# Kernel optimization log

Hardware: AMD Instinct MI355X
Metric: run time of the kernel (lower is better)

The kernel has to match this reference:

```python
import jax, jax.numpy as jnp
import numpy as np

LN_EPS = 1e-5
RMS_EPS = 1e-5

B, T, D = 4, 2048, 1024
H, DK, DV = 4, 256, 512            # head_k_dim = D/H, head_v_dim = expand_v * head_k_dim (expand_v=2)
KDIM, VDIM = H * DK, H * DV        # 1024, 2048
FFN = 4096                          # int(d_model * ffn_ratio)
CONV = 4


def _layernorm(x, w, b):
    mu = jnp.mean(x, -1, keepdims=True)
    var = jnp.mean(jnp.square(x - mu), -1, keepdims=True)
    return (x - mu) * jax.lax.rsqrt(var + LN_EPS) * w + b


def _short_conv_silu(x, w):
    # causal depthwise conv, kernel size K, then SiLU. x: [B,T,C], w: [C,K]
    K = w.shape[1]
    xp = jnp.pad(x, ((0, 0), (K - 1, 0), (0, 0)))
    y = sum(xp[:, i:i + x.shape[1], :] * w[:, i] for i in range(K))
    return jax.nn.silu(y)


def _l2norm(x):
    return x * jax.lax.rsqrt(jnp.sum(jnp.square(x), -1, keepdims=True) + 1e-6)


def _gated_delta_rule(q, k, v, g, beta):
    # q,k: [B,T,H,DK]; v: [B,T,H,DV]; g,beta: [B,T,H]
    # S_t = exp(g_t)*S_{t-1} + k_t (beta_t*(v_t - k_t^T exp(g_t) S_{t-1}))^T ; o_t = q_t^T S_t
    def step(S, inp):
        qt, kt, vt, gt, bt = inp
        S = S * jnp.exp(gt)[..., None, None]          # [B,H,DK,DV]
        mem = jnp.einsum('bhk,bhkv->bhv', kt, S)
        delta = (vt - mem) * bt[..., None]
        S = S + jnp.einsum('bhk,bhv->bhkv', kt, delta)
        o = jnp.einsum('bhk,bhkv->bhv', qt, S)
        return S, o
    S0 = jnp.zeros((q.shape[0], H, DK, DV), q.dtype)
    xs = (q.transpose(1, 0, 2, 3), k.transpose(1, 0, 2, 3), v.transpose(1, 0, 2, 3),
          g.transpose(1, 0, 2), beta.transpose(1, 0, 2))
    _, o = jax.lax.scan(step, S0, xs)
    return o.transpose(1, 0, 2, 3)  # [B,T,H,DV]


def setup_inputs() -> dict:
    key = jax.random.key(0)
    ks = jax.random.split(key, 24)
    n = lambda k, shp, s=0.02: jax.random.normal(k, shp, dtype=jnp.float32) * s
    return {
        'x': jax.random.normal(ks[0], (B, T, D), dtype=jnp.float32),
        'Wq': n(ks[1], (D, KDIM)), 'Wk': n(ks[2], (D, KDIM)), 'Wv': n(ks[3], (D, VDIM)),
        'Wa': n(ks[4], (D, H)), 'Wb': n(ks[5], (D, H)), 'Wg': n(ks[6], (D, VDIM)),
        'conv_q_w': n(ks[7], (KDIM, CONV), 0.2), 'conv_k_w': n(ks[8], (KDIM, CONV), 0.2),
        'conv_v_w': n(ks[9], (VDIM, CONV), 0.2),
        'A_log': jnp.log(jax.random.uniform(ks[10], (H,), minval=1.0, maxval=16.0, dtype=jnp.float32)),
        'dt_bias': jax.random.uniform(ks[11], (H,), minval=0.0, maxval=0.5, dtype=jnp.float32),
        'o_norm_w': jnp.ones((DV,), jnp.float32),
        'Wo': n(ks[12], (VDIM, D)),
        'ln1_w': jnp.ones((D,), jnp.float32), 'ln1_b': jnp.zeros((D,), jnp.float32),
        'ln2_w': jnp.ones((D,), jnp.float32), 'ln2_b': jnp.zeros((D,), jnp.float32),
        'ffn_w1': n(ks[13], (D, FFN)), 'ffn_b1': jnp.zeros((FFN,), jnp.float32),
        'ffn_w2': n(ks[14], (FFN, D)), 'ffn_b2': jnp.zeros((D,), jnp.float32),
    }


def reference(x, Wq, Wk, Wv, Wa, Wb, Wg, conv_q_w, conv_k_w, conv_v_w, A_log, dt_bias,
              o_norm_w, Wo, ln1_w, ln1_b, ln2_w, ln2_b, ffn_w1, ffn_b1, ffn_w2, ffn_b2):
    normed = _layernorm(x, ln1_w, ln1_b)
    q = _short_conv_silu(normed @ Wq, conv_q_w).reshape(B, T, H, DK)
    k = _short_conv_silu(normed @ Wk, conv_k_w).reshape(B, T, H, DK)
    v = _short_conv_silu(normed @ Wv, conv_v_w).reshape(B, T, H, DV)
    q = _l2norm(q) * (DK ** -0.5)
    k = _l2norm(k)
    g = -jnp.exp(A_log) * jax.nn.softplus(normed @ Wa + dt_bias)   # [B,T,H], negative
    beta = jax.nn.sigmoid(normed @ Wb)                              # [B,T,H]
    o = _gated_delta_rule(q, k, v, g, beta)                         # [B,T,H,DV]
    gate = (normed @ Wg).reshape(B, T, H, DV)
    o = o * jax.lax.rsqrt(jnp.mean(jnp.square(o), -1, keepdims=True) + RMS_EPS)
    o = o * o_norm_w * jax.nn.silu(gate)                            # gated RMSNorm
    x = x + o.reshape(B, T, VDIM) @ Wo
    h = _layernorm(x, ln2_w, ln2_b)
    ffn = jax.nn.gelu(h @ ffn_w1 + ffn_b1, approximate=False) @ ffn_w2 + ffn_b2
    return x + ffn
```

## Files before the change

### kernel.cpp

```cpp
#include <hip/hip_runtime.h>
#include <math.h>

#define B_    4
#define T_    2048
#define D_    1024
#define H_    4
#define DK_   256
#define DV_   512
#define KDIM_ 1024
#define VDIM_ 2048
#define FFN_  4096
#define BT_   8192

typedef unsigned short bf16;
typedef __attribute__((ext_vector_type(8))) short short8;
typedef __attribute__((ext_vector_type(4))) short short4v;
typedef __attribute__((ext_vector_type(4))) float f32x4;


__device__ __forceinline__ float sigmoidf_(float x) { return 1.f / (1.f + expf(-x)); }
__device__ __forceinline__ float siluf_(float x)    { return x / (1.f + expf(-x)); }
__device__ __forceinline__ float geluf_(float x)    { return 0.5f * x * (1.f + erff(x * 0.70710678118654752f)); }

__device__ __forceinline__ float bf2f(bf16 u) {
  union { unsigned int i; float f; } c; c.i = (unsigned int)u << 16; return c.f;
}
__device__ __forceinline__ bf16 f2bf(float f) {
  union { unsigned int i; float f; } c; c.f = f;
  unsigned int r = c.i + 0x7fffu + ((c.i >> 16) & 1u);
  return (bf16)(r >> 16);
}

__device__ __forceinline__ void gload16(const bf16* g, bf16* l) {
  __builtin_amdgcn_global_load_lds((__attribute__((address_space(1))) const void*)g,
                                   (__attribute__((address_space(3))) void*)l, 16, 0, 0);
}

__device__ __forceinline__ void storeC(float* p, float v) { *p = v; }
__device__ __forceinline__ void storeC(bf16* p, float v)  { *p = f2bf(v); }

__device__ __forceinline__ short8 ld76(const bf16* p) {
  union { short8 v; short4v h[2]; } u;
  u.h[0] = *(const short4v*)p;
  u.h[1] = *(const short4v*)(p + 4);
  return u.v;
}
__device__ __forceinline__ void st4bf(bf16* p, f32x4 v) {
  short4v o;
  o[0] = (short)f2bf(v[0]); o[1] = (short)f2bf(v[1]);
  o[2] = (short)f2bf(v[2]); o[3] = (short)f2bf(v[3]);
  *(short4v*)p = o;
}

__device__ __forceinline__ float block_sum256(float v, float* red) {
#pragma unroll
  for (int off = 32; off; off >>= 1) v += __shfl_xor(v, off, 64);
  __syncthreads();
  if ((threadIdx.x & 63) == 0) red[threadIdx.x >> 6] = v;
  __syncthreads();
  return red[0] + red[1] + red[2] + red[3];
}


__global__ __launch_bounds__(256) void sentinel_kernel(float* out, int n) {
  int i = blockIdx.x * 256 + threadIdx.x;
  if (i < n) out[i] = 12345.0f;
}


__global__ __launch_bounds__(256) void ln_kernel(const float* __restrict__ x,
                                                 const float* __restrict__ w,
                                                 const float* __restrict__ b,
                                                 bf16* __restrict__ y) {
  __shared__ float red[4];
  int row = blockIdx.x;
  const float* xr = x + (size_t)row * D_;
  float xv[4];
  float s = 0.f;
#pragma unroll
  for (int i = 0; i < 4; i++) { xv[i] = xr[threadIdx.x + 256 * i]; s += xv[i]; }
  float mean = block_sum256(s, red) * (1.f / D_);
  float s2 = 0.f;
#pragma unroll
  for (int i = 0; i < 4; i++) { float d = xv[i] - mean; s2 += d * d; }
  float var = block_sum256(s2, red) * (1.f / D_);
  float inv = rsqrtf(var + 1e-5f);
  bf16* yr = y + (size_t)row * D_;
#pragma unroll
  for (int i = 0; i < 4; i++) {
    int c = threadIdx.x + 256 * i;
    yr[c] = f2bf((xv[i] - mean) * inv * w[c] + b[c]);
  }
}


__global__ __launch_bounds__(256) void convT_kernel(const float* __restrict__ src,
                                                    bf16* __restrict__ dst,
                                                    int K, int N) {
  __shared__ float t[32][33];
  int n0 = blockIdx.x * 32, k0 = blockIdx.y * 32;
  int tx = threadIdx.x & 31, ty = threadIdx.x >> 5;
#pragma unroll
  for (int i = 0; i < 4; i++)
    t[ty + i * 8][tx] = src[(size_t)(k0 + ty + i * 8) * N + n0 + tx];
  __syncthreads();
#pragma unroll
  for (int i = 0; i < 4; i++)
    dst[(size_t)(n0 + ty + i * 8) * K + k0 + tx] = f2bf(t[tx][ty + i * 8]);
}


__global__ __launch_bounds__(256) void kT_kernel(const bf16* __restrict__ k16,
                                                 bf16* __restrict__ kT) {
  __shared__ bf16 tile[32][34];
  int t0 = blockIdx.x * 32;
  int d0 = blockIdx.y * 32;
  int bh = blockIdx.z;
  int b = bh >> 2, h = bh & 3;
  int tx = threadIdx.x & 31, ty = threadIdx.x >> 5;
#pragma unroll
  for (int i = 0; i < 4; i++)
    tile[ty + 8 * i][tx] = k16[(size_t)(b * T_ + t0 + ty + 8 * i) * KDIM_ + h * DK_ + d0 + tx];
  __syncthreads();
  int t = t0 + tx;
  int c = t >> 6, tb = (t >> 3) & 7, te = t & 7;
  size_t base = ((size_t)(bh * 32 + c) * 8 + tb) * 2048 + te;
#pragma unroll
  for (int i = 0; i < 4; i++)
    kT[base + (size_t)(d0 + ty + 8 * i) * 8] = tile[tx][ty + 8 * i];
}


template <typename TC>
__global__ __launch_bounds__(256) void gemm_mfma(const bf16* __restrict__ A,
                                                 const bf16* __restrict__ Bt,
                                                 const float* __restrict__ bias,
                                                 const float* __restrict__ res,
                                                 TC* __restrict__ C,
                                                 int N, int K, int flags) {
  __shared__ __align__(16) bf16 As[3][128 * 32];
  __shared__ __align__(16) bf16 Bs[3][128 * 32];
  int tid = threadIdx.x;
  int wave = tid >> 6, lane = tid & 63;

  int nbx = gridDim.x;
  int id  = blockIdx.y * nbx + blockIdx.x;
  int xcd = id & 7;
  int g   = id >> 3;
  int bx  = g % nbx;
  int by  = xcd + 8 * (g / nbx);
  int bm = by * 128, bn = bx * 128;

  int wm = (wave >> 1) * 64, wn = (wave & 1) * 64;
  int lm = lane & 15;
  int quad = lane >> 4;

  f32x4 acc[4][4];
#pragma unroll
  for (int i = 0; i < 4; i++)
#pragma unroll
    for (int j = 0; j < 4; j++) acc[i][j] = (f32x4){0.f, 0.f, 0.f, 0.f};

  int srow = wave * 32 + (lane >> 2);
  int scol = (lane & 3) * 8;
  const bf16* ag = A  + (size_t)(bm + srow) * K + scol;
  const bf16* bg = Bt + (size_t)(bn + srow) * K + scol;
  const size_t gstep = (size_t)16 * K;
  int woff = wave * 1024;

  int nt = K >> 5;
#pragma unroll
  for (int p = 0; p < 3; p++) {
    int kt = (p < nt) ? p : nt - 1;
    size_t k0 = (size_t)kt << 5;
    gload16(ag + k0,         &As[p][woff]);
    gload16(ag + k0 + gstep, &As[p][woff + 512]);
    gload16(bg + k0,         &Bs[p][woff]);
    gload16(bg + k0 + gstep, &Bs[p][woff + 512]);
  }
  __builtin_amdgcn_sched_barrier(0);

  int cur = 0;
  for (int i = 0; i < nt; i++) {
    asm volatile("s_waitcnt vmcnt(8)" ::: "memory");
    __builtin_amdgcn_s_barrier();
    __builtin_amdgcn_sched_barrier(0);

    short8 af[4], bf[4];
#pragma unroll
    for (int i4 = 0; i4 < 4; i4++)
      af[i4] = *(const short8*)&As[cur][(wm + i4 * 16 + lm) * 32 + quad * 8];
#pragma unroll
    for (int j4 = 0; j4 < 4; j4++)
      bf[j4] = *(const short8*)&Bs[cur][(wn + j4 * 16 + lm) * 32 + quad * 8];
#pragma unroll
    for (int i4 = 0; i4 < 4; i4++)
#pragma unroll
      for (int j4 = 0; j4 < 4; j4++)
        acc[i4][j4] = __builtin_amdgcn_mfma_f32_16x16x32_bf16(af[i4], bf[j4], acc[i4][j4], 0, 0, 0);

    asm volatile("s_waitcnt lgkmcnt(0)" ::: "memory");
    __builtin_amdgcn_s_barrier();
    __builtin_amdgcn_sched_barrier(0);

    {
      int kt = (i + 3 < nt) ? i + 3 : nt - 1;
      size_t k0 = (size_t)kt << 5;
      gload16(ag + k0,         &As[cur][woff]);
      gload16(ag + k0 + gstep, &As[cur][woff + 512]);
      gload16(bg + k0,         &Bs[cur][woff]);
      gload16(bg + k0 + gstep, &Bs[cur][woff + 512]);
    }
    __builtin_amdgcn_sched_barrier(0);

    cur++; if (cur == 3) cur = 0;
  }

#pragma unroll
  for (int i = 0; i < 4; i++) {
    int row0 = bm + wm + i * 16 + quad * 4;
#pragma unroll
    for (int j = 0; j < 4; j++) {
      int col = bn + wn + j * 16 + lm;
      float badd = (flags & 1) ? bias[col] : 0.f;
#pragma unroll
      for (int r = 0; r < 4; r++) {
        float v = acc[i][j][r] + badd;
        if (flags & 2) v = geluf_(v);
        if (flags & 4) v += res[(size_t)(row0 + r) * N + col];
        storeC(&C[(size_t)(row0 + r) * N + col], v);
      }
    }
  }
}


__global__ __launch_bounds__(256) void ab_kernel(const bf16* __restrict__ normed,
                                                 const float* __restrict__ Wa,
                                                 const float* __restrict__ Wb,
                                                 const float* __restrict__ A_log,
                                                 const float* __restrict__ dt_bias,
                                                 float* __restrict__ g,
                                                 float* __restrict__ beta) {
  __shared__ float red[4];
  int row = blockIdx.x;
  const bf16* xr = normed + (size_t)row * D_;
  float aacc[4] = {}, bacc[4] = {};
#pragma unroll
  for (int i = 0; i < 4; i++) {
    int d = threadIdx.x + 256 * i;
    float xv = bf2f(xr[d]);
    float4 wa = *(const float4*)&Wa[d * 4];
    float4 wb = *(const float4*)&Wb[d * 4];
    aacc[0] += xv * wa.x; aacc[1] += xv * wa.y; aacc[2] += xv * wa.z; aacc[3] += xv * wa.w;
    bacc[0] += xv * wb.x; bacc[1] += xv * wb.y; bacc[2] += xv * wb.z; bacc[3] += xv * wb.w;
  }
  float sa[4], sb[4];
#pragma unroll
  for (int h = 0; h < 4; h++) {
    sa[h] = block_sum256(aacc[h], red);
    sb[h] = block_sum256(bacc[h], red);
  }
  if (threadIdx.x < 4) {
    int h = threadIdx.x;
    float xa = sa[h] + dt_bias[h];
    float sp = (xa > 20.f) ? xa : log1pf(expf(xa));
    g[row * 4 + h] = -expf(A_log[h]) * sp;
    beta[row * 4 + h] = sigmoidf_(sb[h]);
  }
}


__global__ __launch_bounds__(256) void conv_qk_kernel(const float* __restrict__ pre,
                                                      const float* __restrict__ convw,
                                                      bf16* __restrict__ out,
                                                      float scale) {
  __shared__ float red[4];
  int blk = blockIdx.x;
  int h = blk & 3;
  int bt = blk >> 2;
  int t = bt & (T_ - 1);
  int c = h * DK_ + threadIdx.x;
  float y = 0.f;
#pragma unroll
  for (int i = 0; i < 4; i++) {
    int tt = t + i - 3;
    if (tt >= 0) y += pre[(size_t)(bt + i - 3) * KDIM_ + c] * convw[c * 4 + i];
  }
  y = siluf_(y);
  float ss = block_sum256(y * y, red);
  y *= rsqrtf(ss + 1e-6f) * scale;
  out[(size_t)bt * KDIM_ + c] = f2bf(y);
}

__global__ __launch_bounds__(256) void conv_v_kernel(const float* __restrict__ pre,
                                                     const float* __restrict__ convw,
                                                     bf16* __restrict__ out) {
  int idx = blockIdx.x * 256 + threadIdx.x;
  int c = idx & (VDIM_ - 1);
  int bt = idx >> 11;
  int t = bt & (T_ - 1);
  float y = 0.f;
#pragma unroll
  for (int i = 0; i < 4; i++) {
    int tt = t + i - 3;
    if (tt >= 0) y += pre[(size_t)(bt + i - 3) * VDIM_ + c] * convw[c * 4 + i];
  }
  out[idx] = f2bf(siluf_(y));
}


#define SP  76
#define UBP 72
#define MTP 68

__global__ __launch_bounds__(256, 2) void delta_p1(const bf16* __restrict__ q,
                                                   const bf16* __restrict__ k,
                                                   const bf16* __restrict__ v,
                                                   const float* __restrict__ g,
                                                   const float* __restrict__ beta,
                                                   bf16* __restrict__ Pg,
                                                   bf16* __restrict__ Wg,
                                                   bf16* __restrict__ Yg,
                                                   float* __restrict__ gsc) {
  __shared__ bf16 Abf[64 * SP];
  __shared__ bf16 DTg[64 * SP];
  __shared__ __align__(8) bf16 MT[64 * MTP];
  __shared__ __align__(8) bf16 Ubt[64 * UBP];
  __shared__ float UbJ[16 * 64];
  __shared__ float Gc[64], Lm[64], Bt[64];

  int blk = blockIdx.x;
  int c = blk & 31, bh = blk >> 5;
  int b = bh >> 2, h = bh & 3;
  int tid = threadIdx.x;
  int wave = tid >> 6, lane = tid & 63;
  int lm = lane & 15, quad = lane >> 4;
  int r0 = c * 64;

  const bf16* kb = k + (size_t)b * T_ * KDIM_ + h * DK_;
  const bf16* qb = q + (size_t)b * T_ * KDIM_ + h * DK_;
  const bf16* vb = v + (size_t)b * T_ * VDIM_ + h * DV_;
  const float* gbp = g    + (size_t)b * T_ * H_ + h;
  const float* bbp = beta + (size_t)b * T_ * H_ + h;
  size_t cb = (size_t)bh * 32 + c;
  bf16* PgC = Pg + cb * 4096;
  bf16* WgC = Wg + cb * 64 * 512;
  bf16* YgC = Yg + cb * 64 * 256;

  if (wave == 0) {
    float gv = gbp[(size_t)(r0 + lane) * H_];
    float bv = bbp[(size_t)(r0 + lane) * H_];
#pragma unroll
    for (int d = 1; d < 64; d <<= 1) {
      float nn = __shfl_up(gv, (unsigned)d, 64);
      if (lane >= d) gv += nn;
    }
    Gc[lane] = gv; Lm[lane] = expf(gv); Bt[lane] = bv;
    gsc[cb * 64 + lane] = gv;
  }
  {
    int* dz = (int*)DTg;
#pragma unroll
    for (int i = 0; i < 10; i++) {
      int idx = tid + 256 * i;
      if (idx < 64 * SP / 2) dz[idx] = 0;
    }
  }
  __syncthreads();

  {
    f32x4 akk[4], aqk[4];
#pragma unroll
    for (int j = 0; j < 4; j++) { akk[j] = (f32x4){0.f,0.f,0.f,0.f}; aqk[j] = (f32x4){0.f,0.f,0.f,0.f}; }
    const bf16* krow = kb + (size_t)(r0 + 16 * wave + lm) * KDIM_;
    const bf16* qrow = qb + (size_t)(r0 + 16 * wave + lm) * KDIM_;
#pragma unroll
    for (int ks = 0; ks < 8; ks++) {
      short8 ak = *(const short8*)(krow + 8 * quad + 32 * ks);
      short8 aq = *(const short8*)(qrow + 8 * quad + 32 * ks);
#pragma unroll
      for (int j = 0; j < 4; j++) {
        short8 bk = *(const short8*)(kb + (size_t)(r0 + 16 * j + lm) * KDIM_ + 8 * quad + 32 * ks);
        akk[j] = __builtin_amdgcn_mfma_f32_16x16x32_bf16(ak, bk, akk[j], 0, 0, 0);
        aqk[j] = __builtin_amdgcn_mfma_f32_16x16x32_bf16(aq, bk, aqk[j], 0, 0, 0);
      }
    }
    float gi[4], bi[4];
#pragma unroll
    for (int r = 0; r < 4; r++) {
      int i = 16 * wave + 4 * quad + r;
      gi[r] = Gc[i]; bi[r] = Bt[i];
    }
#pragma unroll
    for (int j = 0; j < 4; j++) {
      int s = 16 * j + lm;
      float gs = Gc[s];
#pragma unroll
      for (int r = 0; r < 4; r++) {
        int i = 16 * wave + 4 * quad + r;
        float dec = expf(gi[r] - gs);
        Abf[(size_t)i * SP + s] = f2bf((s < i)  ? bi[r] * dec * akk[j][r] : 0.f);
        PgC[(size_t)i * 64 + s] = f2bf((s <= i) ? dec * aqk[j][r]        : 0.f);
      }
    }
  }
  __syncthreads();

#pragma unroll 1
  for (int j = 0; j < 4; j++) {
#pragma unroll
    for (int i = 0; i < 4; i++) {
      int idx = tid + 256 * i;
      int row = idx >> 6, col = idx & 63;
      UbJ[row * 64 + col] = (col == 16 * j + row) ? 1.f : 0.f;
    }
    __syncthreads();
    if (j > 0) {
      f32x4 racc = (f32x4){0.f, 0.f, 0.f, 0.f};
      int nk = (j == 3) ? 2 : 1;
      for (int ks = 0; ks < nk; ks++) {
        short8 aa = ld76(&Abf[(size_t)(16 * j + lm) * SP + 8 * quad + 32 * ks]);
        short8 bd = ld76(&DTg[(size_t)(16 * wave + lm) * SP + 8 * quad + 32 * ks]);
        racc = __builtin_amdgcn_mfma_f32_16x16x32_bf16(aa, bd, racc, 0, 0, 0);
      }
#pragma unroll
      for (int r = 0; r < 4; r++)
        UbJ[(4 * quad + r) * 64 + 16 * wave + lm] -= racc[r];
      __syncthreads();
    }
    if (wave == 0) {
      int tl = lane & 15, sg = lane >> 4;
      short4v ab4 = *(const short4v*)&Abf[(size_t)(16 * j + tl) * SP + 16 * j + 4 * sg];
      float av[4];
      av[0] = bf2f((bf16)ab4[0]); av[1] = bf2f((bf16)ab4[1]);
      av[2] = bf2f((bf16)ab4[2]); av[3] = bf2f((bf16)ab4[3]);
      float d[16];
#pragma unroll
      for (int t = 0; t < 16; t++) {
        float val = UbJ[t * 64 + lane];
#pragma unroll
        for (int s = 0; s < t; s++) {
          float ats = __shfl(av[s & 3], t + 16 * (s >> 2), 64);
          val -= ats * d[s];
        }
        d[t] = val;
        bf16 vb16 = f2bf(val);
        DTg[(size_t)lane * SP + 16 * j + t] = vb16;
        MT [(size_t)(16 * j + t) * MTP + lane] = vb16;
      }
    }
    __syncthreads();
  }

  int cg = 16 * wave + lm;
#pragma unroll 1
  for (int grp = 0; grp < 12; grp++) {
#pragma unroll
    for (int ti = 0; ti < 4; ti++) {
      short4v up;
#pragma unroll
      for (int r = 0; r < 4; r++) {
        int t = 16 * ti + 4 * quad + r;
        float val;
        if (grp < 8) val = Bt[t] * bf2f(vb[(size_t)(r0 + t) * VDIM_ + grp * 64 + cg]);
        else         val = Bt[t] * Lm[t] * bf2f(kb[(size_t)(r0 + t) * KDIM_ + (grp - 8) * 64 + cg]);
        up[r] = (short)f2bf(val);
      }
      *(short4v*)&Ubt[(size_t)cg * UBP + 16 * ti + 4 * quad] = up;
    }
    asm volatile("s_waitcnt lgkmcnt(0)" ::: "memory");
    __builtin_amdgcn_s_barrier();

    f32x4 racc[4];
#pragma unroll
    for (int jt = 0; jt < 4; jt++) racc[jt] = (f32x4){0.f, 0.f, 0.f, 0.f};
#pragma unroll
    for (int ks = 0; ks < 2; ks++) {
      short8 aM = ld76(&MT[(size_t)(16 * wave + lm) * MTP + 8 * quad + 32 * ks]);
#pragma unroll
      for (int jt = 0; jt < 4; jt++) {
        short8 bU = ld76(&Ubt[(size_t)(16 * jt + lm) * UBP + 8 * quad + 32 * ks]);
        racc[jt] = __builtin_amdgcn_mfma_f32_16x16x32_bf16(aM, bU, racc[jt], 0, 0, 0);
      }
    }
#pragma unroll
    for (int jt = 0; jt < 4; jt++) {
#pragma unroll
      for (int rr = 0; rr < 4; rr++) {
        int t = 16 * wave + 4 * quad + rr;
        int cc = 16 * jt + lm;
        if (grp < 8) WgC[(size_t)t * 512 + grp * 64 + cc]       = f2bf(racc[jt][rr]);
        else         YgC[(size_t)t * 256 + (grp - 8) * 64 + cc] = f2bf(racc[jt][rr]);
      }
    }
    asm volatile("s_waitcnt lgkmcnt(0)" ::: "memory");
    __builtin_amdgcn_s_barrier();
  }
}


#define SP2 264
#define SD  72

__global__ __launch_bounds__(256, 1) void delta_p2(const bf16* __restrict__ q,
                                                   const bf16* __restrict__ kT,
                                                   const bf16* __restrict__ Wg,
                                                   const bf16* __restrict__ Yg,
                                                   const bf16* __restrict__ Pg,
                                                   const float* __restrict__ gsc,
                                                   bf16* __restrict__ o) {
  __shared__ __align__(16) bf16 ST[32 * SP2];
  __shared__ __align__(16) bf16 dT[32 * SD];
  __shared__ __align__(16) bf16 dTe[32 * SD];
  __shared__ float Gc[64];
  __shared__ __align__(16) bf16 Ks[2][8 * 256 * 8];
  __shared__ __align__(16) bf16 Ws[2][64 * 32];

  int blk = blockIdx.x;
  int bh = blk & 15, vs = blk >> 4;
  int b = bh >> 2, h = bh & 3;
  int tid = threadIdx.x;
  int wave = tid >> 6, lane = tid & 63;
  int lm = lane & 15, quad = lane >> 4;
  int rt = wave;
  int v0 = vs * 32;

  const bf16* qb  = q  + (size_t)b * T_ * KDIM_ + h * DK_;
  const bf16* kTb = kT + (size_t)bh * 32 * 16384;
  const bf16* WgB = Wg + (size_t)bh * 32 * 32768 + (size_t)(tid >> 2) * 512 + v0 + (tid & 3) * 8;
  const bf16* PgB = Pg + (size_t)bh * 32 * 4096 + (size_t)(16 * rt + lm) * 64 + 8 * quad;
  bf16*       ob  = o  + (size_t)b * T_ * VDIM_ + h * DV_ + v0;

  f32x4 Sacc[4][2];
#pragma unroll
  for (int dd = 0; dd < 4; dd++)
#pragma unroll
    for (int cc = 0; cc < 2; cc++) Sacc[dd][cc] = (f32x4){0.f, 0.f, 0.f, 0.f};

#pragma unroll
  for (int i = 0; i < 8; i++)
    gload16(kTb + i * 2048 + tid * 8, Ks[0] + i * 2048 + wave * 512);
  gload16(WgB, Ws[0] + tid * 8);
  __builtin_amdgcn_sched_barrier(0);
  short8 pfn[2];
  pfn[0] = *(const short8*)(PgB);
  pfn[1] = *(const short8*)(PgB + 32);
  __builtin_amdgcn_sched_barrier(0);
  float gnext = gsc[(size_t)bh * 2048 + lane], gnn = 0.f;
  short8 qfr[8], yfr[8];
  {
    const bf16* qrow = qb + (size_t)(16 * rt + lm) * KDIM_;
    const bf16* yrow = Yg + (size_t)bh * 32 * 16384 + (size_t)(16 * rt + lm) * 256;
#pragma unroll
    for (int kf = 0; kf < 8; kf++) {
      qfr[kf] = *(const short8*)(qrow + 8 * quad + 32 * kf);
      yfr[kf] = *(const short8*)(yrow + 8 * quad + 32 * kf);
    }
  }

  for (int c = 0; c < 32; c++) {
    const int r0 = c * 64;
    const int idx = c & 1;
    const bf16* Ksb = Ks[idx];
    const bf16* Wsb = Ws[idx];
    bf16* Ksn = Ks[idx ^ 1];
    bf16* Wsn = Ws[idx ^ 1];

#pragma unroll
    for (int dd = 0; dd < 4; dd++)
#pragma unroll
      for (int cc = 0; cc < 2; cc++)
        st4bf(&ST[(size_t)(16 * cc + lm) * SP2 + 16 * (4 * wave + dd) + 4 * quad], Sacc[dd][cc]);
    Gc[lane] = gnext;
    asm volatile("s_waitcnt lgkmcnt(0)" ::: "memory");
    __builtin_amdgcn_s_barrier();

    f32x4 Yacc[2], Oacc[2];
#pragma unroll
    for (int cc = 0; cc < 2; cc++) { Yacc[cc] = (f32x4){0.f,0.f,0.f,0.f}; Oacc[cc] = (f32x4){0.f,0.f,0.f,0.f}; }
#pragma unroll
    for (int cc = 0; cc < 2; cc++) {
      short8 Bs2[8];
#pragma unroll
      for (int kf = 0; kf < 8; kf++)
        Bs2[kf] = *(const short8*)&ST[(size_t)(16 * cc + lm) * SP2 + 8 * quad + 32 * kf];
#pragma unroll
      for (int kf = 0; kf < 8; kf++) {
        Yacc[cc] = __builtin_amdgcn_mfma_f32_16x16x32_bf16(yfr[kf], Bs2[kf], Yacc[cc], 0, 0, 0);
        Oacc[cc] = __builtin_amdgcn_mfma_f32_16x16x32_bf16(qfr[kf], Bs2[kf], Oacc[cc], 0, 0, 0);
      }
    }
    __builtin_amdgcn_sched_barrier(0);

    {
      int cn = (c + 1) & 31;
      size_t cbn = (size_t)bh * 32 + cn;
      const bf16* slab = kTb + (size_t)cn * 16384;
#pragma unroll
      for (int i = 0; i < 8; i++)
        gload16(slab + i * 2048 + tid * 8, Ksn + i * 2048 + wave * 512);
      gload16(WgB + (size_t)cn * 32768, Wsn + tid * 8);
      __builtin_amdgcn_sched_barrier(0);
      gnn = gsc[cbn * 64 + lane];
      const bf16* qrow = qb + (size_t)(cn * 64 + 16 * rt + lm) * KDIM_;
      const bf16* yrow = Yg + cbn * 16384 + (size_t)(16 * rt + lm) * 256;
#pragma unroll
      for (int kf = 0; kf < 8; kf++) {
        qfr[kf] = *(const short8*)(qrow + 8 * quad + 32 * kf);
        yfr[kf] = *(const short8*)(yrow + 8 * quad + 32 * kf);
      }
    }
    __builtin_amdgcn_sched_barrier(0);

    asm volatile("" : : "v"(*(const int*)&pfn[0]), "v"(*(const int*)&pfn[1]) : "memory");
    __builtin_amdgcn_sched_barrier(0);
    float g63 = Gc[63];
    float lamv[4], erv[4];
#pragma unroll
    for (int rr = 0; rr < 4; rr++) {
      float gr = Gc[16 * rt + 4 * quad + rr];
      lamv[rr] = __expf(gr);
      erv[rr]  = __expf(g63 - gr);
    }
#pragma unroll
    for (int cc = 0; cc < 2; cc++) {
      short4v dpack, depack;
#pragma unroll
      for (int rr = 0; rr < 4; rr++) {
        int row = 16 * rt + 4 * quad + rr;
        float dv = bf2f(Wsb[row * 32 + 16 * cc + lm]) - Yacc[cc][rr];
        Oacc[cc][rr] *= lamv[rr];
        dpack[rr]  = (short)f2bf(dv);
        depack[rr] = (short)f2bf(dv * erv[rr]);
      }
      *(short4v*)&dT [(size_t)(16 * cc + lm) * SD + 16 * rt + 4 * quad] = dpack;
      *(short4v*)&dTe[(size_t)(16 * cc + lm) * SD + 16 * rt + 4 * quad] = depack;
    }
    asm volatile("s_waitcnt lgkmcnt(0)" ::: "memory");
    __builtin_amdgcn_s_barrier();

    float lend = __expf(g63);
    short8 Be[2][2];
#pragma unroll
    for (int cc = 0; cc < 2; cc++)
#pragma unroll
      for (int kf = 0; kf < 2; kf++)
        Be[cc][kf] = ld76(&dTe[(size_t)(16 * cc + lm) * SD + 8 * quad + 32 * kf]);
#pragma unroll
    for (int dd = 0; dd < 4; dd++) {
      int Dt = 4 * wave + dd;
#pragma unroll
      for (int cc = 0; cc < 2; cc++) {
        f32x4 s = Sacc[dd][cc];
        s[0] *= lend; s[1] *= lend; s[2] *= lend; s[3] *= lend;
#pragma unroll
        for (int kf = 0; kf < 2; kf++) {
          short8 ka = *(const short8*)&Ksb[((size_t)(quad + 4 * kf) * 256 + 16 * Dt + lm) * 8];
          s = __builtin_amdgcn_mfma_f32_16x16x32_bf16(ka, Be[cc][kf], s, 0, 0, 0);
        }
        Sacc[dd][cc] = s;
      }
    }

#pragma unroll
    for (int cc = 0; cc < 2; cc++) {
#pragma unroll
      for (int kf = 0; kf < 2; kf++) {
        short8 bd = ld76(&dT[(size_t)(16 * cc + lm) * SD + 8 * quad + 32 * kf]);
        Oacc[cc] = __builtin_amdgcn_mfma_f32_16x16x32_bf16(pfn[kf], bd, Oacc[cc], 0, 0, 0);
      }
#pragma unroll
      for (int rr = 0; rr < 4; rr++) {
        int row = 16 * rt + 4 * quad + rr;
        ob[(size_t)(r0 + row) * VDIM_ + 16 * cc + lm] = f2bf(Oacc[cc][rr]);
      }
    }
    __builtin_amdgcn_sched_barrier(0);

    {
      int cn = (c + 1) & 31;
      const bf16* pc = PgB + (size_t)cn * 4096;
      pfn[0] = *(const short8*)(pc);
      pfn[1] = *(const short8*)(pc + 32);
    }
    gnext = gnn;
    asm volatile("s_waitcnt lgkmcnt(0)" ::: "memory");
    __builtin_amdgcn_s_barrier();
  }
}


__global__ __launch_bounds__(256) void gated_rms_kernel(bf16* __restrict__ o,
                                                        const bf16* __restrict__ gate,
                                                        const float* __restrict__ onw) {
  __shared__ float red[4];
  int blk = blockIdx.x;
  int h = blk & 3;
  int bt = blk >> 2;
  size_t base = (size_t)bt * VDIM_ + h * DV_;
  int tid = threadIdx.x;
  float o1 = bf2f(o[base + tid]), o2 = bf2f(o[base + tid + 256]);
  float ss = block_sum256(o1 * o1 + o2 * o2, red);
  float s = rsqrtf(ss * (1.f / DV_) + 1e-5f);
  float g1 = bf2f(gate[base + tid]), g2 = bf2f(gate[base + tid + 256]);
  o[base + tid]       = f2bf(o1 * s * onw[tid] * siluf_(g1));
  o[base + tid + 256] = f2bf(o2 * s * onw[tid + 256] * siluf_(g2));
}


extern "C" void kernel_launch(void* const* d_in, const int* in_sizes, int n_in,
                              void* d_out, int out_size, void* d_ws, size_t ws_size,
                              hipStream_t stream) {
  const float* x        = (const float*)d_in[0];
  const float* Wq       = (const float*)d_in[1];
  const float* Wk       = (const float*)d_in[2];
  const float* Wv       = (const float*)d_in[3];
  const float* Wa       = (const float*)d_in[4];
  const float* Wb       = (const float*)d_in[5];
  const float* Wg       = (const float*)d_in[6];
  const float* conv_q_w = (const float*)d_in[7];
  const float* conv_k_w = (const float*)d_in[8];
  const float* conv_v_w = (const float*)d_in[9];
  const float* A_log    = (const float*)d_in[10];
  const float* dt_bias  = (const float*)d_in[11];
  const float* o_norm_w = (const float*)d_in[12];
  const float* Wo       = (const float*)d_in[13];
  const float* ln1_w    = (const float*)d_in[14];
  const float* ln1_b    = (const float*)d_in[15];
  const float* ln2_w    = (const float*)d_in[16];
  const float* ln2_b    = (const float*)d_in[17];
  const float* ffn_w1   = (const float*)d_in[18];
  const float* ffn_b1   = (const float*)d_in[19];
  const float* ffn_w2   = (const float*)d_in[20];
  const float* ffn_b2   = (const float*)d_in[21];

  size_t required = (size_t)218 << 20;
  if (ws_size < required) {
    sentinel_kernel<<<(out_size + 255) / 256, 256, 0, stream>>>((float*)d_out, out_size);
    return;
  }

  char* base = (char*)d_ws;
  float* pre    = (float*)(base);
  bf16*  normed = (bf16*)(base + ((size_t)64  << 20));
  bf16*  q16    = (bf16*)(base + ((size_t)80  << 20));
  bf16*  k16    = (bf16*)(base + ((size_t)96  << 20));
  bf16*  v16    = (bf16*)(base + ((size_t)112 << 20));
  bf16*  g16    = (bf16*)(base + ((size_t)144 << 20));
  bf16*  o16    = (bf16*)(base + ((size_t)176 << 20));
  bf16*  wslot  = (bf16*)(base + ((size_t)208 << 20));
  float* gvec   = (float*)(base + ((size_t)216 << 20));
  float* bvec   = gvec + (size_t)BT_ * H_;
  float* gsc    = (float*)(base + ((size_t)217 << 20));
  bf16*  Yg     = (bf16*)(base);
  bf16*  Wgb    = (bf16*)(base + ((size_t)16 << 20));
  bf16*  Pg     = (bf16*)(base + ((size_t)48 << 20));
  bf16*  kTg    = (bf16*)(base + ((size_t)52 << 20));
  float* x2     = (float*)(base);
  bf16*  hb16   = (bf16*)(base + ((size_t)64  << 20));
  bf16*  ffn1   = (bf16*)(base + ((size_t)80  << 20));

  ln_kernel<<<BT_, 256, 0, stream>>>(x, ln1_w, ln1_b, normed);

  convT_kernel<<<dim3(KDIM_ / 32, D_ / 32), 256, 0, stream>>>(Wq, wslot, D_, KDIM_);
  gemm_mfma<float><<<dim3(KDIM_ / 128, BT_ / 128), 256, 0, stream>>>(normed, wslot, nullptr, nullptr, pre, KDIM_, D_, 0);
  conv_qk_kernel<<<BT_ * H_, 256, 0, stream>>>(pre, conv_q_w, q16, 0.0625f);

  convT_kernel<<<dim3(KDIM_ / 32, D_ / 32), 256, 0, stream>>>(Wk, wslot, D_, KDIM_);
  gemm_mfma<float><<<dim3(KDIM_ / 128, BT_ / 128), 256, 0, stream>>>(normed, wslot, nullptr, nullptr, pre, KDIM_, D_, 0);
  conv_qk_kernel<<<BT_ * H_, 256, 0, stream>>>(pre, conv_k_w, k16, 1.0f);

  convT_kernel<<<dim3(VDIM_ / 32, D_ / 32), 256, 0, stream>>>(Wv, wslot, D_, VDIM_);
  gemm_mfma<float><<<dim3(VDIM_ / 128, BT_ / 128), 256, 0, stream>>>(normed, wslot, nullptr, nullptr, pre, VDIM_, D_, 0);
  conv_v_kernel<<<(BT_ * VDIM_) / 256, 256, 0, stream>>>(pre, conv_v_w, v16);

  convT_kernel<<<dim3(VDIM_ / 32, D_ / 32), 256, 0, stream>>>(Wg, wslot, D_, VDIM_);
  gemm_mfma<bf16><<<dim3(VDIM_ / 128, BT_ / 128), 256, 0, stream>>>(normed, wslot, nullptr, nullptr, g16, VDIM_, D_, 0);

  ab_kernel<<<BT_, 256, 0, stream>>>(normed, Wa, Wb, A_log, dt_bias, gvec, bvec);

  kT_kernel<<<dim3(T_ / 32, DK_ / 32, 16), 256, 0, stream>>>(k16, kTg);
  delta_p1<<<512, 256, 0, stream>>>(q16, k16, v16, gvec, bvec, Pg, Wgb, Yg, gsc);
  delta_p2<<<256, 256, 0, stream>>>(q16, kTg, Wgb, Yg, Pg, gsc, o16);

  gated_rms_kernel<<<BT_ * H_, 256, 0, stream>>>(o16, g16, o_norm_w);

  convT_kernel<<<dim3(D_ / 32, VDIM_ / 32), 256, 0, stream>>>(Wo, wslot, VDIM_, D_);
  gemm_mfma<float><<<dim3(D_ / 128, BT_ / 128), 256, 0, stream>>>(o16, wslot, nullptr, x, x2, D_, VDIM_, 4);

  ln_kernel<<<BT_, 256, 0, stream>>>(x2, ln2_w, ln2_b, hb16);

  convT_kernel<<<dim3(FFN_ / 32, D_ / 32), 256, 0, stream>>>(ffn_w1, wslot, D_, FFN_);
  gemm_mfma<bf16><<<dim3(FFN_ / 128, BT_ / 128), 256, 0, stream>>>(hb16, wslot, ffn_b1, nullptr, ffn1, FFN_, D_, 1 | 2);
  convT_kernel<<<dim3(D_ / 32, FFN_ / 32), 256, 0, stream>>>(ffn_w2, wslot, FFN_, D_);
  gemm_mfma<float><<<dim3(D_ / 128, BT_ / 128), 256, 0, stream>>>(ffn1, wslot, ffn_b2, x2, (float*)d_out, D_, FFN_, 1 | 4);
}
```

Measured before the change: 1.045 ms.

## Add 256x256-tile double-buffered MFMA GEMM for wide-N projections

Introduces a new 512-thread GEMM kernel with 256x256 output tiles, 8 waves each computing 128x64, double-buffered LDS with swizzled layout and an XCD-aware block remap. It replaces the 128x128 GEMM for the V, gate, and FFN-up projections, raising arithmetic intensity per loaded byte. The larger tile uses 128KB LDS and many accumulator registers at one block per CU, and the grids become small (e.g. 256 blocks), which risks poorer CU occupancy and latency hiding.

New measurement: 1.028 ms. No clear change (-1.6%).

```diff
diff --git a/kernel.cpp b/kernel.cpp
--- a/kernel.cpp
+++ b/kernel.cpp
@@ -226,6 +226,114 @@
 #pragma unroll
       for (int r = 0; r < 4; r++) {
         float v = acc[i][j][r] + badd;
+        if (flags & 2) v = geluf_(v);
+        if (flags & 4) v += res[(size_t)(row0 + r) * N + col];
+        storeC(&C[(size_t)(row0 + r) * N + col], v);
+      }
+    }
+  }
+}
+
+
+template <typename TC>
+__global__ __launch_bounds__(512, 1) void gemm256(const bf16* __restrict__ A,
+                                                  const bf16* __restrict__ Bt,
+                                                  const float* __restrict__ bias,
+                                                  const float* __restrict__ res,
+                                                  TC* __restrict__ C,
+                                                  int N, int K, int flags) {
+  __shared__ __align__(16) bf16 As[2][256 * 64];
+  __shared__ __align__(16) bf16 Bs[2][256 * 64];
+  int tid = threadIdx.x;
+  int wave = tid >> 6, lane = tid & 63;
+  int lm = lane & 15, quad = lane >> 4;
+  int wm8 = wave >> 2, wn8 = wave & 3;
+
+  int nbx = gridDim.x;
+  int id  = blockIdx.y * nbx + blockIdx.x;
+  int xcd = id & 7;
+  int g   = id >> 3;
+  int bx  = g % nbx;
+  int by  = xcd + 8 * (g / nbx);
+  int bm = by * 256, bn = bx * 256;
+
+  f32x4 acc[8][4];
+#pragma unroll
+  for (int i = 0; i < 8; i++)
+#pragma unroll
+    for (int j = 0; j < 4; j++) acc[i][j] = (f32x4){0.f, 0.f, 0.f, 0.f};
+
+  int srow = tid >> 3;
+  int scol = ((tid & 7) ^ (srow & 7)) * 8;
+  const bf16* agb = A  + (size_t)(bm + srow) * K + scol;
+  const bf16* bgb = Bt + (size_t)(bn + srow) * K + scol;
+  const size_t rstep = (size_t)64 * K;
+  int ldst = tid * 8;
+
+  int nt = K >> 6;
+#pragma unroll
+  for (int p = 0; p < 2; p++) {
+    size_t k0 = (size_t)p << 6;
+#pragma unroll
+    for (int r = 0; r < 4; r++) {
+      gload16(agb + r * rstep + k0, (bf16*)As[p] + r * 4096 + ldst);
+      gload16(bgb + r * rstep + k0, (bf16*)Bs[p] + r * 4096 + ldst);
+    }
+  }
+  __builtin_amdgcn_sched_barrier(0);
+
+  int cur = 0;
+  for (int i = 0; i < nt; i++) {
+    asm volatile("s_waitcnt vmcnt(8)" ::: "memory");
+    __builtin_amdgcn_s_barrier();
+    __builtin_amdgcn_sched_barrier(0);
+
+    const bf16* Ab = As[cur];
+    const bf16* Bb = Bs[cur];
+#pragma unroll
+    for (int kk = 0; kk < 2; kk++) {
+      int colr = (8 * quad + 32 * kk) ^ ((lm & 7) << 3);
+      short8 af[8], bfr[4];
+#pragma unroll
+      for (int i8 = 0; i8 < 8; i8++)
+        af[i8] = *(const short8*)&Ab[(wm8 * 128 + i8 * 16 + lm) * 64 + colr];
+#pragma unroll
+      for (int j4 = 0; j4 < 4; j4++)
+        bfr[j4] = *(const short8*)&Bb[(wn8 * 64 + j4 * 16 + lm) * 64 + colr];
+#pragma unroll
+      for (int i8 = 0; i8 < 8; i8++)
+#pragma unroll
+        for (int j4 = 0; j4 < 4; j4++)
+          acc[i8][j4] = __builtin_amdgcn_mfma_f32_16x16x32_bf16(af[i8], bfr[j4], acc[i8][j4], 0, 0, 0);
+    }
+
+    asm volatile("s_waitcnt lgkmcnt(0)" ::: "memory");
+    __builtin_amdgcn_s_barrier();
+    __builtin_amdgcn_sched_barrier(0);
+
+    {
+      int kt = (i + 2 < nt) ? i + 2 : nt - 1;
+      size_t k0 = (size_t)kt << 6;
+#pragma unroll
+      for (int r = 0; r < 4; r++) {
+        gload16(agb + r * rstep + k0, (bf16*)As[cur] + r * 4096 + ldst);
+        gload16(bgb + r * rstep + k0, (bf16*)Bs[cur] + r * 4096 + ldst);
+      }
+    }
+    __builtin_amdgcn_sched_barrier(0);
+    cur ^= 1;
+  }
+
+#pragma unroll
+  for (int i8 = 0; i8 < 8; i8++) {
+    int row0 = bm + wm8 * 128 + i8 * 16 + quad * 4;
+#pragma unroll
+    for (int j4 = 0; j4 < 4; j4++) {
+      int col = bn + wn8 * 64 + j4 * 16 + lm;
+      float badd = (flags & 1) ? bias[col] : 0.f;
+#pragma unroll
+      for (int r = 0; r < 4; r++) {
+        float v = acc[i8][j4][r] + badd;
         if (flags & 2) v = geluf_(v);
         if (flags & 4) v += res[(size_t)(row0 + r) * N + col];
         storeC(&C[(size_t)(row0 + r) * N + col], v);
@@ -772,11 +880,11 @@
   conv_qk_kernel<<<BT_ * H_, 256, 0, stream>>>(pre, conv_k_w, k16, 1.0f);
 
   convT_kernel<<<dim3(VDIM_ / 32, D_ / 32), 256, 0, stream>>>(Wv, wslot, D_, VDIM_);
-  gemm_mfma<float><<<dim3(VDIM_ / 128, BT_ / 128), 256, 0, stream>>>(normed, wslot, nullptr, nullptr, pre, VDIM_, D_, 0);
+  gemm256<float><<<dim3(VDIM_ / 256, BT_ / 256), 512, 0, stream>>>(normed, wslot, nullptr, nullptr, pre, VDIM_, D_, 0);
   conv_v_kernel<<<(BT_ * VDIM_) / 256, 256, 0, stream>>>(pre, conv_v_w, v16);
 
   convT_kernel<<<dim3(VDIM_ / 32, D_ / 32), 256, 0, stream>>>(Wg, wslot, D_, VDIM_);
-  gemm_mfma<bf16><<<dim3(VDIM_ / 128, BT_ / 128), 256, 0, stream>>>(normed, wslot, nullptr, nullptr, g16, VDIM_, D_, 0);
+  gemm256<bf16><<<dim3(VDIM_ / 256, BT_ / 256), 512, 0, stream>>>(normed, wslot, nullptr, nullptr, g16, VDIM_, D_, 0);
 
   ab_kernel<<<BT_, 256, 0, stream>>>(normed, Wa, Wb, A_log, dt_bias, gvec, bvec);
 
@@ -792,7 +900,7 @@
   ln_kernel<<<BT_, 256, 0, stream>>>(x2, ln2_w, ln2_b, hb16);
 
   convT_kernel<<<dim3(FFN_ / 32, D_ / 32), 256, 0, stream>>>(ffn_w1, wslot, D_, FFN_);
-  gemm_mfma<bf16><<<dim3(FFN_ / 128, BT_ / 128), 256, 0, stream>>>(hb16, wslot, ffn_b1, nullptr, ffn1, FFN_, D_, 1 | 2);
+  gemm256<bf16><<<dim3(FFN_ / 256, BT_ / 256), 512, 0, stream>>>(hb16, wslot, ffn_b1, nullptr, ffn1, FFN_, D_, 1 | 2);
   convT_kernel<<<dim3(D_ / 32, FFN_ / 32), 256, 0, stream>>>(ffn_w2, wslot, FFN_, D_);
   gemm_mfma<float><<<dim3(D_ / 128, BT_ / 128), 256, 0, stream>>>(ffn1, wslot, ffn_b2, x2, (float*)d_out, D_, FFN_, 1 | 4);
 }
```

## Replace 128x128 GEMM with 256-row tiles, K=64 steps and swizzled LDS

Applied to the files above, without the earlier changes.

Replaces the GEMM kernel with a templated 512-thread version that uses 256-row by 128- or 256-column output tiles, a K step of 64 with double buffering instead of triple buffering, and an XOR-swizzled LDS layout meant to avoid bank conflicts. The larger tiles raise arithmetic intensity and data reuse per block, and the swizzle cuts LDS conflicts on fragment reads. In exchange, each block uses more LDS and registers, occupancy is forced to one block per SM, and the grid has fewer blocks, which may underfill the GPU for the N=1024 GEMMs.

After: 1.137 ms. +8.8%, slower.

```diff
diff --git a/kernel.cpp b/kernel.cpp
--- a/kernel.cpp
+++ b/kernel.cpp
@@ -131,17 +131,23 @@
 }
 
 
-template <typename TC>
-__global__ __launch_bounds__(256) void gemm_mfma(const bf16* __restrict__ A,
-                                                 const bf16* __restrict__ Bt,
-                                                 const float* __restrict__ bias,
-                                                 const float* __restrict__ res,
-                                                 TC* __restrict__ C,
-                                                 int N, int K, int flags) {
-  __shared__ __align__(16) bf16 As[3][128 * 32];
-  __shared__ __align__(16) bf16 Bs[3][128 * 32];
+template <typename TC, int BN, int WM, int WN>
+__global__ __launch_bounds__(512, 1) void gemm256t(const bf16* __restrict__ A,
+                                                   const bf16* __restrict__ Bt,
+                                                   const float* __restrict__ bias,
+                                                   const float* __restrict__ res,
+                                                   TC* __restrict__ C,
+                                                   int N, int K, int flags) {
+  constexpr int MI = 256 / WM / 16;
+  constexpr int NJ = BN / WN / 16;
+  constexpr int BR = BN / 64;
+  constexpr int LOADS = 4 + BR;
+  __shared__ __align__(16) bf16 As[2][256 * 64];
+  __shared__ __align__(16) bf16 Bs[2][BN * 64];
   int tid = threadIdx.x;
   int wave = tid >> 6, lane = tid & 63;
+  int lm = lane & 15, quad = lane >> 4;
+  int wmi = wave / WN, wnj = wave % WN;
 
   int nbx = gridDim.x;
   int id  = blockIdx.y * nbx + blockIdx.x;
@@ -149,83 +155,88 @@
   int g   = id >> 3;
   int bx  = g % nbx;
   int by  = xcd + 8 * (g / nbx);
-  int bm = by * 128, bn = bx * 128;
-
-  int wm = (wave >> 1) * 64, wn = (wave & 1) * 64;
-  int lm = lane & 15;
-  int quad = lane >> 4;
-
-  f32x4 acc[4][4];
-#pragma unroll
-  for (int i = 0; i < 4; i++)
-#pragma unroll
-    for (int j = 0; j < 4; j++) acc[i][j] = (f32x4){0.f, 0.f, 0.f, 0.f};
-
-  int srow = wave * 32 + (lane >> 2);
-  int scol = (lane & 3) * 8;
-  const bf16* ag = A  + (size_t)(bm + srow) * K + scol;
-  const bf16* bg = Bt + (size_t)(bn + srow) * K + scol;
-  const size_t gstep = (size_t)16 * K;
-  int woff = wave * 1024;
-
-  int nt = K >> 5;
-#pragma unroll
-  for (int p = 0; p < 3; p++) {
-    int kt = (p < nt) ? p : nt - 1;
-    size_t k0 = (size_t)kt << 5;
-    gload16(ag + k0,         &As[p][woff]);
-    gload16(ag + k0 + gstep, &As[p][woff + 512]);
-    gload16(bg + k0,         &Bs[p][woff]);
-    gload16(bg + k0 + gstep, &Bs[p][woff + 512]);
+  int bm = by * 256, bn = bx * BN;
+
+  f32x4 acc[MI][NJ];
+#pragma unroll
+  for (int i = 0; i < MI; i++)
+#pragma unroll
+    for (int j = 0; j < NJ; j++) acc[i][j] = (f32x4){0.f, 0.f, 0.f, 0.f};
+
+  int srow = tid >> 3;
+  int scol = ((tid & 7) ^ (srow & 7)) * 8;
+  const bf16* agb = A  + (size_t)(bm + srow) * K + scol;
+  const bf16* bgb = Bt + (size_t)(bn + srow) * K + scol;
+  const size_t rstep = (size_t)64 * K;
+  int ldst = tid * 8;
+
+  int nt = K >> 6;
+#pragma unroll
+  for (int p = 0; p < 2; p++) {
+    size_t k0 = (size_t)p << 6;
+#pragma unroll
+    for (int r = 0; r < 4; r++)
+      gload16(agb + r * rstep + k0, (bf16*)As[p] + r * 4096 + ldst);
+#pragma unroll
+    for (int r = 0; r < BR; r++)
+      gload16(bgb + r * rstep + k0, (bf16*)Bs[p] + r * 4096 + ldst);
   }
   __builtin_amdgcn_sched_barrier(0);
 
   int cur = 0;
   for (int i = 0; i < nt; i++) {
-    asm volatile("s_waitcnt vmcnt(8)" ::: "memory");
+    if constexpr (LOADS == 8) asm volatile("s_waitcnt vmcnt(8)" ::: "memory");
+    else                      asm volatile("s_waitcnt vmcnt(6)" ::: "memory");
     __builtin_amdgcn_s_barrier();
     __builtin_amdgcn_sched_barrier(0);
 
-    short8 af[4], bf[4];
-#pragma unroll
-    for (int i4 = 0; i4 < 4; i4++)
-      af[i4] = *(const short8*)&As[cur][(wm + i4 * 16 + lm) * 32 + quad * 8];
-#pragma unroll
-    for (int j4 = 0; j4 < 4; j4++)
-      bf[j4] = *(const short8*)&Bs[cur][(wn + j4 * 16 + lm) * 32 + quad * 8];
-#pragma unroll
-    for (int i4 = 0; i4 < 4; i4++)
-#pragma unroll
-      for (int j4 = 0; j4 < 4; j4++)
-        acc[i4][j4] = __builtin_amdgcn_mfma_f32_16x16x32_bf16(af[i4], bf[j4], acc[i4][j4], 0, 0, 0);
+    const bf16* Ab = As[cur];
+    const bf16* Bb = Bs[cur];
+#pragma unroll
+    for (int kk = 0; kk < 2; kk++) {
+      int colr = (8 * quad + 32 * kk) ^ ((lm & 7) << 3);
+      short8 af[MI], bfr[NJ];
+#pragma unroll
+      for (int i8 = 0; i8 < MI; i8++)
+        af[i8] = *(const short8*)&Ab[(wmi * MI * 16 + i8 * 16 + lm) * 64 + colr];
+#pragma unroll
+      for (int j4 = 0; j4 < NJ; j4++)
+        bfr[j4] = *(const short8*)&Bb[(wnj * NJ * 16 + j4 * 16 + lm) * 64 + colr];
+#pragma unroll
+      for (int i8 = 0; i8 < MI; i8++)
+#pragma unroll
+        for (int j4 = 0; j4 < NJ; j4++)
+          acc[i8][j4] = __builtin_amdgcn_mfma_f32_16x16x32_bf16(af[i8], bfr[j4], acc[i8][j4], 0, 0, 0);
+    }
 
     asm volatile("s_waitcnt lgkmcnt(0)" ::: "memory");
     __builtin_amdgcn_s_barrier();
     __builtin_amdgcn_sched_barrier(0);
 
     {
-      int kt = (i + 3 < nt) ? i + 3 : nt - 1;
-      size_t k0 = (size_t)kt << 5;
-      gload16(ag + k0,         &As[cur][woff]);
-      gload16(ag + k0 + gstep, &As[cur][woff + 512]);
-      gload16(bg + k0,         &Bs[cur][woff]);
-      gload16(bg + k0 + gstep, &Bs[cur][woff + 512]);
+      int kt = (i + 2 < nt) ? i + 2 : nt - 1;
+      size_t k0 = (size_t)kt << 6;
+#pragma unroll
+      for (int r = 0; r < 4; r++)
+        gload16(agb + r * rstep + k0, (bf16*)As[cur] + r * 4096 + ldst);
+#pragma unroll
+      for (int r = 0; r < BR; r++)
+        gload16(bgb + r * rstep + k0, (bf16*)Bs[cur] + r * 4096 + ldst);
     }
     __builtin_amdgcn_sched_barrier(0);
-
-    cur++; if (cur == 3) cur = 0;
-  }
-
-#pragma unroll
-  for (int i = 0; i < 4; i++) {
-    int row0 = bm + wm + i * 16 + quad * 4;
-#pragma unroll
-    for (int j = 0; j < 4; j++) {
-      int col = bn + wn + j * 16 + lm;
+    cur ^= 1;
+  }
+
+#pragma unroll
+  for (int i8 = 0; i8 < MI; i8++) {
+    int row0 = bm + wmi * MI * 16 + i8 * 16 + quad * 4;
+#pragma unroll
+    for (int j4 = 0; j4 < NJ; j4++) {
+      int col = bn + wnj * NJ * 16 + j4 * 16 + lm;
       float badd = (flags & 1) ? bias[col] : 0.f;
 #pragma unroll
       for (int r = 0; r < 4; r++) {
-        float v = acc[i][j][r] + badd;
+        float v = acc[i8][j4][r] + badd;
         if (flags & 2) v = geluf_(v);
         if (flags & 4) v += res[(size_t)(row0 + r) * N + col];
         storeC(&C[(size_t)(row0 + r) * N + col], v);
@@ -764,19 +775,19 @@
   ln_kernel<<<BT_, 256, 0, stream>>>(x, ln1_w, ln1_b, normed);
 
   convT_kernel<<<dim3(KDIM_ / 32, D_ / 32), 256, 0, stream>>>(Wq, wslot, D_, KDIM_);
-  gemm_mfma<float><<<dim3(KDIM_ / 128, BT_ / 128), 256, 0, stream>>>(normed, wslot, nullptr, nullptr, pre, KDIM_, D_, 0);
+  gemm256t<float, 128, 4, 2><<<dim3(KDIM_ / 128, BT_ / 256), 512, 0, stream>>>(normed, wslot, nullptr, nullptr, pre, KDIM_, D_, 0);
   conv_qk_kernel<<<BT_ * H_, 256, 0, stream>>>(pre, conv_q_w, q16, 0.0625f);
 
   convT_kernel<<<dim3(KDIM_ / 32, D_ / 32), 256, 0, stream>>>(Wk, wslot, D_, KDIM_);
-  gemm_mfma<float><<<dim3(KDIM_ / 128, BT_ / 128), 256, 0, stream>>>(normed, wslot, nullptr, nullptr, pre, KDIM_, D_, 0);
+  gemm256t<float, 128, 4, 2><<<dim3(KDIM_ / 128, BT_ / 256), 512, 0, stream>>>(normed, wslot, nullptr, nullptr, pre, KDIM_, D_, 0);
   conv_qk_kernel<<<BT_ * H_, 256, 0, stream>>>(pre, conv_k_w, k16, 1.0f);
 
   convT_kernel<<<dim3(VDIM_ / 32, D_ / 32), 256, 0, stream>>>(Wv, wslot, D_, VDIM_);
-  gemm_mfma<float><<<dim3(VDIM_ / 128, BT_ / 128), 256, 0, stream>>>(normed, wslot, nullptr, nullptr, pre, VDIM_, D_, 0);
+  gemm256t<float, 256, 2, 4><<<dim3(VDIM_ / 256, BT_ / 256), 512, 0, stream>>>(normed, wslot, nullptr, nullptr, pre, VDIM_, D_, 0);
   conv_v_kernel<<<(BT_ * VDIM_) / 256, 256, 0, stream>>>(pre, conv_v_w, v16);
 
   convT_kernel<<<dim3(VDIM_ / 32, D_ / 32), 256, 0, stream>>>(Wg, wslot, D_, VDIM_);
-  gemm_mfma<bf16><<<dim3(VDIM_ / 128, BT_ / 128), 256, 0, stream>>>(normed, wslot, nullptr, nullptr, g16, VDIM_, D_, 0);
+  gemm256t<bf16, 256, 2, 4><<<dim3(VDIM_ / 256, BT_ / 256), 512, 0, stream>>>(normed, wslot, nullptr, nullptr, g16, VDIM_, D_, 0);
 
   ab_kernel<<<BT_, 256, 0, stream>>>(normed, Wa, Wb, A_log, dt_bias, gvec, bvec);
 
@@ -787,12 +798,12 @@
   gated_rms_kernel<<<BT_ * H_, 256, 0, stream>>>(o16, g16, o_norm_w);
 
   convT_kernel<<<dim3(D_ / 32, VDIM_ / 32), 256, 0, stream>>>(Wo, wslot, VDIM_, D_);
-  gemm_mfma<float><<<dim3(D_ / 128, BT_ / 128), 256, 0, stream>>>(o16, wslot, nullptr, x, x2, D_, VDIM_, 4);
+  gemm256t<float, 128, 4, 2><<<dim3(D_ / 128, BT_ / 256), 512, 0, stream>>>(o16, wslot, nullptr, x, x2, D_, VDIM_, 4);
 
   ln_kernel<<<BT_, 256, 0, stream>>>(x2, ln2_w, ln2_b, hb16);
 
   convT_kernel<<<dim3(FFN_ / 32, D_ / 32), 256, 0, stream>>>(ffn_w1, wslot, D_, FFN_);
-  gemm_mfma<bf16><<<dim3(FFN_ / 128, BT_ / 128), 256, 0, stream>>>(hb16, wslot, ffn_b1, nullptr, ffn1, FFN_, D_, 1 | 2);
+  gemm256t<bf16, 256, 2, 4><<<dim3(FFN_ / 256, BT_ / 256), 512, 0, stream>>>(hb16, wslot, ffn_b1, nullptr, ffn1, FFN_, D_, 1 | 2);
   convT_kernel<<<dim3(D_ / 32, FFN_ / 32), 256, 0, stream>>>(ffn_w2, wslot, FFN_, D_);
-  gemm_mfma<float><<<dim3(D_ / 128, BT_ / 128), 256, 0, stream>>>(ffn1, wslot, ffn_b2, x2, (float*)d_out, D_, FFN_, 1 | 4);
-}
+  gemm256t<float, 128, 4, 2><<<dim3(D_ / 128, BT_ / 256), 512, 0, stream>>>(ffn1, wslot, ffn_b2, x2, (float*)d_out, D_, FFN_, 1 | 4);
+}
```
